# Performance work log

Measured on AMD Instinct MI355X. Metric: run time of the kernel, lower is better.

Reference implementation:

```python
import jax, jax.numpy as jnp
import numpy as np

N_ADDR, N_TX = 150000, 200000
IN_DIM, HID, HEADS = 64, 32, 4
DIM = HID // HEADS
E_AT, E_TA, E_AA = 1000000, 1000000, 500000
SLOPE = 0.2  # HANConv default negative_slope


def setup_inputs() -> dict:
    key = jax.random.key(0)
    ks = jax.random.split(key, 16)
    f = lambda k, shape, s: jax.random.normal(k, shape, dtype=jnp.float32) * s
    return {
        "x_addr": f(ks[0], (N_ADDR, IN_DIM), 1.0),
        "x_tx": f(ks[1], (N_TX, IN_DIM), 1.0),
        "e_at_src": jax.random.randint(ks[2], (E_AT,), 0, N_ADDR, dtype=jnp.int32),
        "e_at_dst": jax.random.randint(ks[3], (E_AT,), 0, N_TX, dtype=jnp.int32),
        "e_ta_src": jax.random.randint(ks[4], (E_TA,), 0, N_TX, dtype=jnp.int32),
        "e_ta_dst": jax.random.randint(ks[5], (E_TA,), 0, N_ADDR, dtype=jnp.int32),
        "e_aa_src": jax.random.randint(ks[6], (E_AA,), 0, N_ADDR, dtype=jnp.int32),
        "e_aa_dst": jax.random.randint(ks[7], (E_AA,), 0, N_ADDR, dtype=jnp.int32),
        "pW1": f(ks[8], (2, IN_DIM, HID), 0.1),      # layer-1 proj per node type [addr, tx]
        "pb1": jnp.zeros((2, HID), jnp.float32),
        "pW23": f(ks[9], (2, 2, HID, HID), 0.1),     # [layer-1, node_type]
        "pb23": jnp.zeros((2, 2, HID), jnp.float32),
        "att_src": f(ks[10], (3, 3, HEADS, DIM), 0.1),  # [layer, edge_type, H, D]
        "att_dst": f(ks[11], (3, 3, HEADS, DIM), 0.1),
        "kW": f(ks[12], (3, HID, HID), 0.1),         # semantic k_lin per layer
        "kb": jnp.zeros((3, HID), jnp.float32),
        "q": f(ks[13], (3, HID), 0.1),               # semantic query per layer
        "linW": f(ks[14], (HID, 2), 0.1),
        "linb": jnp.zeros((2,), jnp.float32),
    }


def _edge_softmax(logits, dst, n):
    # numerically stable segment softmax over destination neighborhoods
    m = jax.ops.segment_max(logits, dst, num_segments=n)          # [n, H]
    m = jnp.where(jnp.isfinite(m), m, 0.0)
    e = jnp.exp(logits - m[dst])
    s = jax.ops.segment_sum(e, dst, num_segments=n)
    return e / (s[dst] + 1e-16)


def _relation(h_src, h_dst, src, dst, a_s, a_d, n_dst):
    alpha_src = jnp.einsum('nhd,hd->nh', h_src, a_s)
    alpha_dst = jnp.einsum('nhd,hd->nh', h_dst, a_d)
    logit = alpha_src[src] + alpha_dst[dst]                        # [E, H]
    logit = jnp.where(logit >= 0, logit, SLOPE * logit)            # leaky_relu
    alpha = _edge_softmax(logit, dst, n_dst)
    msg = h_src[src] * alpha[:, :, None]                           # [E, H, D]
    out = jax.ops.segment_sum(msg, dst, num_segments=n_dst)        # [n_dst, H, D]
    return jax.nn.relu(out.reshape(n_dst, HID))


def _semantic(xs, kW, kb, q):
    # xs: [R, N, F]; semantic-level attention over R relations (PyG `group`)
    t = jnp.tanh(xs @ kW + kb).mean(axis=1)       # [R, F]
    attn = jax.nn.softmax((t * q).sum(-1))        # [R]
    return jnp.einsum('r,rnf->nf', attn, xs)


def _han_layer(x_a, x_t, Wa, ba, Wt, bt, a_s, a_d, kW, kb, q, edges):
    h_a = (x_a @ Wa + ba).reshape(-1, HEADS, DIM)
    h_t = (x_t @ Wt + bt).reshape(-1, HEADS, DIM)
    o_tx = _relation(h_a, h_t, edges[0], edges[1], a_s[0], a_d[0], N_TX)
    o_a1 = _relation(h_t, h_a, edges[2], edges[3], a_s[1], a_d[1], N_ADDR)
    o_a2 = _relation(h_a, h_a, edges[4], edges[5], a_s[2], a_d[2], N_ADDR)
    new_a = _semantic(jnp.stack([o_a1, o_a2]), kW, kb, q)
    new_t = _semantic(o_tx[None], kW, kb, q)
    return new_a, new_t


def reference(x_addr, x_tx, e_at_src, e_at_dst, e_ta_src, e_ta_dst,
              e_aa_src, e_aa_dst, pW1, pb1, pW23, pb23, att_src, att_dst,
              kW, kb, q, linW, linb):
    edges = (e_at_src, e_at_dst, e_ta_src, e_ta_dst, e_aa_src, e_aa_dst)
    a, t = _han_layer(x_addr, x_tx, pW1[0], pb1[0], pW1[1], pb1[1],
                      att_src[0], att_dst[0], kW[0], kb[0], q[0], edges)
    a, t = jax.nn.relu(a), jax.nn.relu(t)  # wrapper relu; dropout = eval identity
    for l in range(2):
        a, t = _han_layer(a, t, pW23[l, 0], pb23[l, 0], pW23[l, 1], pb23[l, 1],
                          att_src[l + 1], att_dst[l + 1],
                          kW[l + 1], kb[l + 1], q[l + 1], edges)
        a, t = jax.nn.relu(a), jax.nn.relu(t)
    return a @ linW + linb
```

## Files before the change

### kernel.cpp

```cpp
#include <hip/hip_runtime.h>
#include <hip/hip_bf16.h>
#include <hip/hip_fp16.h>

#define NA 150000
#define NT 200000
#define E_AT 1000000
#define E_TA 1000000
#define E_AA 500000

#define CHK 2048
#define CAP 8192
#define P_AT 391
#define P_TA 293
#define P_AA 293
#define NBINS (P_AT + P_TA + P_AA)
#define CB_AT 489
#define CB_TA 489
#define CB_AA 245

#define GB_AT 6250
#define GB_TA 4688
#define GB_AA 4688

#define GA32 4688
#define GT32 6250
#define NB_SEM 586

#define WO_W1   0
#define WO_B1   4096
#define WO_W23  4160
#define WO_B23  8256
#define WO_AS   8384
#define WO_AD   8672
#define WO_KW   8960
#define WO_KB   12032
#define WO_Q    12128
#define WO_LW   12224
#define WO_LB   12288
#define WT_TOT  12290

__device__ __forceinline__ float ldf(const void* p, long i, int f32) {
    if (f32) return ((const float*)p)[i];
    unsigned int u = ((const unsigned short*)p)[i];
    union { unsigned int ui; float f; } v; v.ui = u << 16;
    return v.f;
}
__device__ __forceinline__ float bf2f(unsigned short u) {
    union { unsigned int ui; float f; } v; v.ui = ((unsigned int)u) << 16;
    return v.f;
}
__device__ __forceinline__ float h2f(unsigned short u) {
    return __half2float(__ushort_as_half(u));
}
__device__ __forceinline__ unsigned short f2h(float x) {
    return __half_as_ushort(__float2half(x));
}
__device__ __forceinline__ float ftanh(float x) {
    x = fminf(fmaxf(x, -9.f), 9.f);
    float e = __expf(2.f * x);
    return (e - 1.f) / (e + 1.f);
}

__global__ void k_init(const void* __restrict__ x,
                       const void* __restrict__ pW1, const void* __restrict__ pb1,
                       const void* __restrict__ pW23, const void* __restrict__ pb23,
                       const void* __restrict__ attS, const void* __restrict__ attD,
                       const void* __restrict__ kW, const void* __restrict__ kb,
                       const void* __restrict__ qv, const void* __restrict__ linW,
                       const void* __restrict__ linb,
                       float* __restrict__ wts, int* __restrict__ flagp,
                       int* __restrict__ gcnt) {
    __shared__ int cnt;
    const int t = threadIdx.x;
    if (t == 0) cnt = 0;
    __syncthreads();
    const unsigned short* u = (const unsigned short*)x;
    int wild = 0;
    for (int i = t; i < 4096; i += 256) {
        unsigned short v = u[i];
        int e = (v >> 7) & 0xFF;
        if (e > 133 || (e != 0 && e < 100)) wild++;
        else if (e == 0 && (v & 0x7F)) wild++;
    }
    atomicAdd(&cnt, wild);
    __syncthreads();
    const int f32 = (cnt > 1024) ? 1 : 0;
    if (t == 0) *flagp = f32;
    for (int i = t; i < 1024; i += 256) gcnt[i] = 0;
    for (int i = t; i < 4096; i += 256) wts[WO_W1 + i]  = ldf(pW1, i, f32);
    for (int i = t; i < 64;   i += 256) wts[WO_B1 + i]  = ldf(pb1, i, f32);
    for (int i = t; i < 4096; i += 256) wts[WO_W23 + i] = ldf(pW23, i, f32);
    for (int i = t; i < 128;  i += 256) wts[WO_B23 + i] = ldf(pb23, i, f32);
    for (int i = t; i < 288;  i += 256) wts[WO_AS + i]  = ldf(attS, i, f32);
    for (int i = t; i < 288;  i += 256) wts[WO_AD + i]  = ldf(attD, i, f32);
    for (int i = t; i < 3072; i += 256) wts[WO_KW + i]  = ldf(kW, i, f32);
    for (int i = t; i < 96;   i += 256) wts[WO_KB + i]  = ldf(kb, i, f32);
    for (int i = t; i < 96;   i += 256) wts[WO_Q + i]   = ldf(qv, i, f32);
    for (int i = t; i < 64;   i += 256) wts[WO_LW + i]  = ldf(linW, i, f32);
    for (int i = t; i < 2;    i += 256) wts[WO_LB + i]  = ldf(linb, i, f32);
}

template<int K, int LMODE>
__global__ __launch_bounds__(256) void k_proj2(
        const void* __restrict__ Xa, const void* __restrict__ Xt,
        const void* __restrict__ X2, const float* __restrict__ attn,
        const float* __restrict__ W, int wOffA, int wOffT,
        const float* __restrict__ Bv, int bOffA, int bOffT,
        unsigned short* __restrict__ Ha, unsigned short* __restrict__ Ht,
        const float* __restrict__ attD, int lBase,
        float* __restrict__ ad0, float* __restrict__ ad1, float* __restrict__ ad2,
        const int* __restrict__ flagp, float* __restrict__ zsem) {
    constexpr int XS = K + 4;
    constexpr int CPR = K / 4;
    constexpr int TOT4 = 32 * CPR;
    __shared__ float Xs[32 * XS];
    __shared__ float Wl[K * 32];
    const int t = threadIdx.x;
    if (blockIdx.x == 0 && t < 64) zsem[t] = 0.f;
    const bool isA = blockIdx.x < GA32;
    const int bb = isA ? (int)blockIdx.x : (int)blockIdx.x - GA32;
    const int N = isA ? NA : NT;
    const int wOff = isA ? wOffA : wOffT;
    const int bOff = isA ? bOffA : bOffT;
    const long n0 = (long)bb * 32;
    for (int i = t; i < K * 32; i += 256) Wl[i] = W[wOff + i];
    if (LMODE == 1) {
        if (isA) {
            const float w0 = attn[0], w1 = attn[1];
            const float* A1 = (const float*)Xa;
            const float* A2 = (const float*)X2;
            for (int i = t; i < TOT4; i += 256) {
                int r = i / CPR, c = (i - r * CPR) * 4;
                long gr = n0 + r; if (gr >= N) gr = N - 1;
                float4 va = *(const float4*)&A1[gr * K + c];
                float4 vb = *(const float4*)&A2[gr * K + c];
                float4 o;
                o.x = fmaxf(w0 * va.x + w1 * vb.x, 0.f);
                o.y = fmaxf(w0 * va.y + w1 * vb.y, 0.f);
                o.z = fmaxf(w0 * va.z + w1 * vb.z, 0.f);
                o.w = fmaxf(w0 * va.w + w1 * vb.w, 0.f);
                *(float4*)&Xs[r * XS + c] = o;
            }
        } else {
            const float* Xf = (const float*)Xt;
            for (int i = t; i < TOT4; i += 256) {
                int r = i / CPR, c = (i - r * CPR) * 4;
                long gr = n0 + r; if (gr >= N) gr = N - 1;
                *(float4*)&Xs[r * XS + c] = *(const float4*)&Xf[gr * K + c];
            }
        }
    } else {
        const void* X = isA ? Xa : Xt;
        const int f32 = *flagp;
        if (f32) {
            const float* Xf = (const float*)X;
            for (int i = t; i < TOT4; i += 256) {
                int r = i / CPR, c = (i - r * CPR) * 4;
                long gr = n0 + r; if (gr >= N) gr = N - 1;
                *(float4*)&Xs[r * XS + c] = *(const float4*)&Xf[gr * K + c];
            }
        } else {
            const unsigned short* Xh = (const unsigned short*)X;
            for (int i = t; i < TOT4; i += 256) {
                int r = i / CPR, c = (i - r * CPR) * 4;
                long gr = n0 + r; if (gr >= N) gr = N - 1;
                ushort4 v = *(const ushort4*)&Xh[gr * K + c];
                float4 o;
                o.x = bf2f(v.x); o.y = bf2f(v.y); o.z = bf2f(v.z); o.w = bf2f(v.w);
                *(float4*)&Xs[r * XS + c] = o;
            }
        }
    }
    __syncthreads();
    const int g = t >> 3;
    const int q = t & 7;
    const long n = n0 + g;
    float a0 = Bv[bOff + q * 4 + 0];
    float a1 = Bv[bOff + q * 4 + 1];
    float a2 = Bv[bOff + q * 4 + 2];
    float a3 = Bv[bOff + q * 4 + 3];
#pragma unroll 4
    for (int k4 = 0; k4 < K; k4 += 4) {
        float4 xv = *(const float4*)&Xs[g * XS + k4];
        float4 w0 = *(const float4*)&Wl[(k4 + 0) * 32 + q * 4];
        float4 w1 = *(const float4*)&Wl[(k4 + 1) * 32 + q * 4];
        float4 w2 = *(const float4*)&Wl[(k4 + 2) * 32 + q * 4];
        float4 w3 = *(const float4*)&Wl[(k4 + 3) * 32 + q * 4];
        a0 = fmaf(xv.x, w0.x, a0); a1 = fmaf(xv.x, w0.y, a1);
        a2 = fmaf(xv.x, w0.z, a2); a3 = fmaf(xv.x, w0.w, a3);
        a0 = fmaf(xv.y, w1.x, a0); a1 = fmaf(xv.y, w1.y, a1);
        a2 = fmaf(xv.y, w1.z, a2); a3 = fmaf(xv.y, w1.w, a3);
        a0 = fmaf(xv.z, w2.x, a0); a1 = fmaf(xv.z, w2.y, a1);
        a2 = fmaf(xv.z, w2.z, a2); a3 = fmaf(xv.z, w2.w, a3);
        a0 = fmaf(xv.w, w3.x, a0); a1 = fmaf(xv.w, w3.y, a1);
        a2 = fmaf(xv.w, w3.z, a2); a3 = fmaf(xv.w, w3.w, a3);
    }
    if (n < N) {
        unsigned short* Hh = isA ? Ha : Ht;
        unsigned int p01 = (unsigned)f2h(a0) | ((unsigned)f2h(a1) << 16);
        unsigned int p23 = (unsigned)f2h(a2) | ((unsigned)f2h(a3) << 16);
        *(uint2*)&Hh[n * 32 + q * 4] = make_uint2(p01, p23);
        const int hh = q >> 1;
        const int ai = lBase + q * 4;
        if (isA) {
            float p1 = a0 * attD[ai + 32] + a1 * attD[ai + 33]
                     + a2 * attD[ai + 34] + a3 * attD[ai + 35];
            float p2 = a0 * attD[ai + 64] + a1 * attD[ai + 65]
                     + a2 * attD[ai + 66] + a3 * attD[ai + 67];
            float s1 = p1 + __shfl_xor(p1, 1);
            float s2 = p2 + __shfl_xor(p2, 1);
            if (!(q & 1)) { ad1[n * 4 + hh] = s1; ad2[n * 4 + hh] = s2; }
        } else {
            float p0 = a0 * attD[ai] + a1 * attD[ai + 1]
                     + a2 * attD[ai + 2] + a3 * attD[ai + 3];
            float s0 = p0 + __shfl_xor(p0, 1);
            if (!(q & 1)) ad0[n * 4 + hh] = s0;
        }
    }
}

__global__ __launch_bounds__(256) void k_bin(
        const int* __restrict__ eat_s, const int* __restrict__ eat_d,
        const int* __restrict__ eta_s, const int* __restrict__ eta_d,
        const int* __restrict__ eaa_s, const int* __restrict__ eaa_d,
        int* __restrict__ gcnt,
        int* __restrict__ slot_at, int* __restrict__ slot_ta, int* __restrict__ slot_aa) {
    __shared__ int hist[P_AT];
    int b = blockIdx.x, t = threadIdx.x;
    const int *src, *dst; int E, P, seg; int* slot;
    if (b < CB_AT)              { src = eat_s; dst = eat_d; E = E_AT; P = P_AT; seg = 0;            slot = slot_at; }
    else if (b < CB_AT + CB_TA) { b -= CB_AT;  src = eta_s; dst = eta_d; E = E_TA; P = P_TA; seg = P_AT;        slot = slot_ta; }
    else                        { b -= CB_AT + CB_TA; src = eaa_s; dst = eaa_d; E = E_AA; P = P_AA; seg = P_AT + P_TA; slot = slot_aa; }
    long e0 = (long)b * CHK;
    for (int i = t; i < P; i += 256) hist[i] = 0;
    __syncthreads();
    for (int k = 0; k < CHK; k += 256) {
        long e = e0 + k + t;
        if (e < E) atomicAdd(&hist[dst[e] >> 9], 1);
    }
    __syncthreads();
    for (int i = t; i < P; i += 256) {
        int v = hist[i];
        hist[i] = atomicAdd(&gcnt[seg + i], v);
    }
    __syncthreads();
    for (int k = 0; k < CHK; k += 256) {
        long e = e0 + k + t;
        if (e < E) {
            int d = dst[e];
            int bin = d >> 9;
            int pos = atomicAdd(&hist[bin], 1);
            slot[bin * CAP + pos] = ((d & 511) << 18) | src[e];
        }
    }
}

__global__ void k_binscan(const int* __restrict__ gcnt, int* __restrict__ bbase,
                          int* __restrict__ off_at, int* __restrict__ off_ta,
                          int* __restrict__ off_aa) {
    __shared__ int sa[512], sb[512];
    int t = threadIdx.x;
    const int segs[4] = {0, P_AT, P_AT + P_TA, NBINS};
    for (int r = 0; r < 3; r++) {
        int s0 = segs[r], P = segs[r + 1] - s0;
        sa[t] = (t < P) ? gcnt[s0 + t] : 0;
        __syncthreads();
        int* in = sa; int* out = sb;
        for (int o = 1; o < 512; o <<= 1) {
            out[t] = in[t] + (t >= o ? in[t - o] : 0);
            __syncthreads();
            int* tmp = in; in = out; out = tmp;
        }
        if (t < P) bbase[s0 + t] = (t ? in[t - 1] : 0);
        __syncthreads();
    }
    if (t == 0) { off_at[NT] = E_AT; off_ta[NA] = E_TA; off_aa[NA] = E_AA; }
}

__global__ __launch_bounds__(256) void k_binsort(
        const int* __restrict__ gcnt, const int* __restrict__ bbase,
        const int* __restrict__ slot_at, const int* __restrict__ slot_ta,
        const int* __restrict__ slot_aa,
        int* __restrict__ off_at, int* __restrict__ off_ta, int* __restrict__ off_aa,
        int* __restrict__ csr_at, int* __restrict__ csr_ta, int* __restrict__ csr_aa) {
    __shared__ int sa[512], sb[512], cur[512];
    int b = blockIdx.x, t = threadIdx.x;
    const int* slot; int* off; int* csr; int N, bin, seg;
    if (b < P_AT)              { slot = slot_at; off = off_at; csr = csr_at; N = NT; bin = b;                seg = 0; }
    else if (b < P_AT + P_TA)  { slot = slot_ta; off = off_ta; csr = csr_ta; N = NA; bin = b - P_AT;         seg = P_AT; }
    else                       { slot = slot_aa; off = off_aa; csr = csr_aa; N = NA; bin = b - P_AT - P_TA;  seg = P_AT + P_TA; }
    const int cnt  = gcnt[seg + bin];
    const int base = bbase[seg + bin];
    const int* sp = &slot[bin * CAP];
    sa[t] = 0; sa[t + 256] = 0;
    __syncthreads();
    for (int i = t; i < cnt; i += 256) atomicAdd(&sa[sp[i] >> 18], 1);
    __syncthreads();
    int* in = sa; int* out = sb;
    for (int o = 1; o < 512; o <<= 1) {
        for (int i = t; i < 512; i += 256)
            out[i] = in[i] + (i >= o ? in[i - o] : 0);
        __syncthreads();
        int* tmp = in; in = out; out = tmp;
    }
    for (int i = t; i < 512; i += 256) {
        int excl = i ? in[i - 1] : 0;
        cur[i] = excl;
        int gd = bin * 512 + i;
        if (gd < N) off[gd] = base + excl;
    }
    __syncthreads();
    for (int i = t; i < cnt; i += 256) {
        int pk = sp[i];
        int pos = atomicAdd(&cur[pk >> 18], 1);
        csr[base + pos] = pk & 0x3FFFF;
    }
}

__global__ __launch_bounds__(256) void k_gather3(
        const int* __restrict__ off_at, const int* __restrict__ csr_at,
        const int* __restrict__ off_ta, const int* __restrict__ csr_ta,
        const int* __restrict__ off_aa, const int* __restrict__ csr_aa,
        const float* __restrict__ ad0, const float* __restrict__ ad1,
        const float* __restrict__ ad2,
        const unsigned short* __restrict__ h_a, const unsigned short* __restrict__ h_t,
        float* __restrict__ o_tx, float* __restrict__ o_a1, float* __restrict__ o_a2,
        const float* __restrict__ attS, int lBase) {
    int b = blockIdx.x;
    const int *off, *csr;
    const float *ad_;
    const unsigned short* Hs;
    float* O;
    int N, attOff;
    if (b < GB_AT) {
        off = off_at; csr = csr_at; ad_ = ad0; Hs = h_a; O = o_tx; N = NT;
        attOff = lBase;
    } else if (b < GB_AT + GB_TA) {
        b -= GB_AT;
        off = off_ta; csr = csr_ta; ad_ = ad1; Hs = h_t; O = o_a1; N = NA;
        attOff = lBase + 32;
    } else {
        b -= GB_AT + GB_TA;
        off = off_aa; csr = csr_aa; ad_ = ad2; Hs = h_a; O = o_a2; N = NA;
        attOff = lBase + 64;
    }
    const int t = threadIdx.x;
    const int q = t & 7;
    const int hh = q >> 1;
    const int n = b * 32 + (t >> 3);
    if (n >= N) return;
    const float4 aq = *(const float4*)&attS[attOff + q * 4];
    const float aq0 = aq.x, aq1 = aq.y, aq2 = aq.z, aq3 = aq.w;
    const float adv = ad_[n * 4 + hh];
    const int p0 = off[n], p1 = off[n + 1];
    float ax = 0.f, ay = 0.f, az = 0.f, aw = 0.f, se = 0.f;
    int p = p0;
    for (; p + 4 <= p1; p += 4) {
        int s0 = csr[p], s1 = csr[p + 1], s2 = csr[p + 2], s3 = csr[p + 3];
        ushort4 v0 = *(const ushort4*)&Hs[s0 * 32 + q * 4];
        ushort4 v1 = *(const ushort4*)&Hs[s1 * 32 + q * 4];
        ushort4 v2 = *(const ushort4*)&Hs[s2 * 32 + q * 4];
        ushort4 v3 = *(const ushort4*)&Hs[s3 * 32 + q * 4];
        float h00 = h2f(v0.x), h01 = h2f(v0.y), h02 = h2f(v0.z), h03 = h2f(v0.w);
        float h10 = h2f(v1.x), h11 = h2f(v1.y), h12 = h2f(v1.z), h13 = h2f(v1.w);
        float h20 = h2f(v2.x), h21 = h2f(v2.y), h22 = h2f(v2.z), h23 = h2f(v2.w);
        float h30 = h2f(v3.x), h31 = h2f(v3.y), h32 = h2f(v3.z), h33 = h2f(v3.w);
        float pt0 = h00 * aq0 + h01 * aq1 + h02 * aq2 + h03 * aq3;
        float pt1 = h10 * aq0 + h11 * aq1 + h12 * aq2 + h13 * aq3;
        float pt2 = h20 * aq0 + h21 * aq1 + h22 * aq2 + h23 * aq3;
        float pt3 = h30 * aq0 + h31 * aq1 + h32 * aq2 + h33 * aq3;
        float al0 = pt0 + __shfl_xor(pt0, 1);
        float al1 = pt1 + __shfl_xor(pt1, 1);
        float al2 = pt2 + __shfl_xor(pt2, 1);
        float al3 = pt3 + __shfl_xor(pt3, 1);
        float l0 = al0 + adv; l0 = fmaxf(l0, 0.2f * l0); float e0 = __expf(l0);
        float l1 = al1 + adv; l1 = fmaxf(l1, 0.2f * l1); float e1 = __expf(l1);
        float l2 = al2 + adv; l2 = fmaxf(l2, 0.2f * l2); float e2 = __expf(l2);
        float l3 = al3 + adv; l3 = fmaxf(l3, 0.2f * l3); float e3 = __expf(l3);
        se += e0 + e1 + e2 + e3;
        ax += e0 * h00 + e1 * h10 + e2 * h20 + e3 * h30;
        ay += e0 * h01 + e1 * h11 + e2 * h21 + e3 * h31;
        az += e0 * h02 + e1 * h12 + e2 * h22 + e3 * h32;
        aw += e0 * h03 + e1 * h13 + e2 * h23 + e3 * h33;
    }
    for (; p < p1; p++) {
        int s = csr[p];
        ushort4 v = *(const ushort4*)&Hs[s * 32 + q * 4];
        float h0 = h2f(v.x), h1 = h2f(v.y), h2 = h2f(v.z), h3 = h2f(v.w);
        float pt = h0 * aq0 + h1 * aq1 + h2 * aq2 + h3 * aq3;
        float al = pt + __shfl_xor(pt, 1);
        float l = al + adv; l = fmaxf(l, 0.2f * l);
        float e = __expf(l);
        se += e;
        ax += e * h0; ay += e * h1; az += e * h2; aw += e * h3;
    }
    const float inv = 1.f / (se + 1e-16f);
    float4 r;
    r.x = fmaxf(ax * inv, 0.f);
    r.y = fmaxf(ay * inv, 0.f);
    r.z = fmaxf(az * inv, 0.f);
    r.w = fmaxf(aw * inv, 0.f);
    *(float4*)&O[n * 32 + q * 4] = r;
}

__global__ __launch_bounds__(256) void k_sem_reduce2(
        const float* __restrict__ O1, const float* __restrict__ O2,
        const float* __restrict__ kWl, const float* __restrict__ kbl,
        float* __restrict__ accum) {
    __shared__ float w[1056];
    __shared__ float sacc[32];
    const int r = (blockIdx.x >= NB_SEM) ? 1 : 0;
    const float* O = r ? O2 : O1;
    for (int i = threadIdx.x; i < 1024; i += 256) w[i] = kWl[i];
    if (threadIdx.x < 32) {
        w[1024 + threadIdx.x] = kbl[threadIdx.x];
        sacc[threadIdx.x] = 0.f;
    }
    __syncthreads();
    long n = (long)(blockIdx.x - r * NB_SEM) * 256 + threadIdx.x;
    float y[32];
    if (n < NA) {
        float x[32];
#pragma unroll
        for (int k = 0; k < 32; k++) x[k] = O[n * 32 + k];
#pragma unroll
        for (int f = 0; f < 32; f++) {
            float acc = w[1024 + f];
#pragma unroll
            for (int k = 0; k < 32; k++) acc += x[k] * w[k * 32 + f];
            y[f] = ftanh(acc);
        }
    } else {
#pragma unroll
        for (int f = 0; f < 32; f++) y[f] = 0.f;
    }
#pragma unroll
    for (int f = 0; f < 32; f++) {
        float v = y[f];
        for (int o = 32; o > 0; o >>= 1) v += __shfl_xor(v, o, 64);
        if ((threadIdx.x & 63) == 0) atomicAdd(&sacc[f], v);
    }
    __syncthreads();
    if (threadIdx.x < 32) atomicAdd(&accum[r * 32 + threadIdx.x], sacc[threadIdx.x]);
}

__global__ void k_sem_attn(const float* __restrict__ accum, float Ninv,
                           const float* __restrict__ q, float* __restrict__ attn) {
    if (threadIdx.x == 0) {
        float s0 = 0.f, s1 = 0.f;
        for (int f = 0; f < 32; f++) {
            float qf = q[f];
            s0 += accum[f] * Ninv * qf;
            s1 += accum[32 + f] * Ninv * qf;
        }
        float m = fmaxf(s0, s1);
        float e0 = __expf(s0 - m), e1 = __expf(s1 - m);
        float inv = 1.f / (e0 + e1);
        attn[0] = e0 * inv;
        attn[1] = e1 * inv;
    }
}

__global__ void k_combine_final(const float* __restrict__ o1, const float* __restrict__ o2,
                                const float* __restrict__ attn,
                                const float* __restrict__ linW, const float* __restrict__ linb,
                                void* __restrict__ out, int N, const int* __restrict__ flagp) {
    int n = blockIdx.x * blockDim.x + threadIdx.x;
    if (n >= N) return;
    int f32 = *flagp;
    float w0 = attn[0], w1 = attn[1];
    float s0 = linb[0], s1 = linb[1];
    const float* p1 = &o1[(long)n * 32];
    const float* p2 = &o2[(long)n * 32];
#pragma unroll
    for (int f = 0; f < 32; f++) {
        float v = w0 * p1[f] + w1 * p2[f];
        v = (v > 0.f) ? v : 0.f;
        s0 += v * linW[f * 2];
        s1 += v * linW[f * 2 + 1];
    }
    if (f32) { ((float*)out)[n * 2] = s0; ((float*)out)[n * 2 + 1] = s1; }
    else {
        ((__hip_bfloat16*)out)[n * 2] = __float2bfloat16(s0);
        ((__hip_bfloat16*)out)[n * 2 + 1] = __float2bfloat16(s1);
    }
}

static inline int gblocks(long n) { return (int)((n + 255) / 256); }

extern "C" void kernel_launch(void* const* d_in, const int* in_sizes, int n_in,
                              void* d_out, int out_size, void* d_ws, size_t ws_size,
                              hipStream_t stream) {
    const void* x_addr = d_in[0];
    const void* x_tx   = d_in[1];
    const int* eat_s = (const int*)d_in[2];
    const int* eat_d = (const int*)d_in[3];
    const int* eta_s = (const int*)d_in[4];
    const int* eta_d = (const int*)d_in[5];
    const int* eaa_s = (const int*)d_in[6];
    const int* eaa_d = (const int*)d_in[7];
    const void* pW1  = d_in[8];
    const void* pb1  = d_in[9];
    const void* pW23 = d_in[10];
    const void* pb23 = d_in[11];
    const void* attS = d_in[12];
    const void* attD = d_in[13];
    const void* kW   = d_in[14];
    const void* kb   = d_in[15];
    const void* qv   = d_in[16];
    const void* linW = d_in[17];
    const void* linb = d_in[18];

    const size_t NA32 = (size_t)NA * 32, NT32 = (size_t)NT * 32;
    const size_t NA4 = (size_t)NA * 4, NT4 = (size_t)NT * 4;

    float* ws    = (float*)d_ws;
    float* h_aF  = ws;
    float* h_tF  = h_aF + NA32;
    float* o_a1  = h_tF + NT32;
    float* o_a2  = o_a1 + NA32;
    float* o_tx  = o_a2 + NA32;
    float* ad1   = o_tx + NT32;
    float* ad2   = ad1 + NA4;
    float* ad0   = ad2 + NA4;
    float* sem   = ad0 + NT4;
    int*   flagp = (int*)(sem + 66);
    int*   off_at = flagp + 16;
    int*   off_ta = off_at + (NT + 1);
    int*   off_aa = off_ta + (NA + 1);
    int*   csr_at = off_aa + (NA + 1);
    int*   csr_ta = csr_at + E_AT;
    int*   csr_aa = csr_ta + E_TA;
    int*   gcnt   = csr_aa + E_AA;
    int*   bbase  = gcnt + 1024;
    int*   slot_at = bbase + 1024;
    int*   slot_ta = slot_at + P_AT * CAP;
    int*   slot_aa = slot_ta + P_TA * CAP;
    float* wts    = (float*)(slot_aa + (size_t)P_AA * CAP);

    unsigned short* h_a = (unsigned short*)h_aF;
    unsigned short* h_t = (unsigned short*)h_tF;

    k_init<<<1, 256, 0, stream>>>(x_addr, pW1, pb1, pW23, pb23, attS, attD,
                                  kW, kb, qv, linW, linb, wts, flagp, gcnt);

    k_bin<<<CB_AT + CB_TA + CB_AA, 256, 0, stream>>>(
        eat_s, eat_d, eta_s, eta_d, eaa_s, eaa_d, gcnt, slot_at, slot_ta, slot_aa);
    k_binscan<<<1, 512, 0, stream>>>(gcnt, bbase, off_at, off_ta, off_aa);
    k_binsort<<<NBINS, 256, 0, stream>>>(gcnt, bbase, slot_at, slot_ta, slot_aa,
                                         off_at, off_ta, off_aa, csr_at, csr_ta, csr_aa);

    for (int l = 0; l < 3; l++) {
        if (l == 0) {
            k_proj2<64, 0><<<GA32 + GT32, 256, 0, stream>>>(
                x_addr, x_tx, nullptr, sem + 64,
                wts + WO_W1, 0, 2048, wts + WO_B1, 0, 32,
                h_a, h_t, wts + WO_AD, 0, ad0, ad1, ad2, flagp, sem);
        } else {
            int wi = (l - 1) * 2;
            k_proj2<32, 1><<<GA32 + GT32, 256, 0, stream>>>(
                o_a1, o_tx, o_a2, sem + 64,
                wts + WO_W23, (wi + 0) * 1024, (wi + 1) * 1024,
                wts + WO_B23, (wi + 0) * 32, (wi + 1) * 32,
                h_a, h_t, wts + WO_AD, l * 96, ad0, ad1, ad2, flagp, sem);
        }
        k_gather3<<<GB_AT + GB_TA + GB_AA, 256, 0, stream>>>(
            off_at, csr_at, off_ta, csr_ta, off_aa, csr_aa,
            ad0, ad1, ad2, h_a, h_t, o_tx, o_a1, o_a2, wts + WO_AS, l * 96);
        k_sem_reduce2<<<2 * NB_SEM, 256, 0, stream>>>(
            o_a1, o_a2, wts + WO_KW + l * 1024, wts + WO_KB + l * 32, sem);
        k_sem_attn<<<1, 64, 0, stream>>>(sem, 1.0f / NA, wts + WO_Q + l * 32, sem + 64);
        if (l == 2) {
            k_combine_final<<<gblocks(NA), 256, 0, stream>>>(o_a1, o_a2, sem + 64,
                                                             wts + WO_LW, wts + WO_LB,
                                                             d_out, NA, flagp);
        }
    }
}
```

Before: 662.4 us.

## Fuse semantic attention into gather and edge binning into layer-1 projection

After: 780.9 us. +17.9%, slower.

```diff
diff --git a/kernel.cpp b/kernel.cpp
--- a/kernel.cpp
+++ b/kernel.cpp
@@ -8,15 +8,16 @@
 #define E_TA 1000000
 #define E_AA 500000
 
-#define CHK 2048
+#define CHK 4096
 #define CAP 8192
 #define P_AT 391
 #define P_TA 293
 #define P_AA 293
 #define NBINS (P_AT + P_TA + P_AA)
-#define CB_AT 489
-#define CB_TA 489
-#define CB_AA 245
+#define CB_AT 245
+#define CB_TA 245
+#define CB_AA 123
+#define NBBIN (CB_AT + CB_TA + CB_AA)
 
 #define GB_AT 6250
 #define GB_TA 4688
@@ -24,7 +25,6 @@
 
 #define GA32 4688
 #define GT32 6250
-#define NB_SEM 586
 
 #define WO_W1   0
 #define WO_B1   4096
@@ -37,7 +37,6 @@
 #define WO_Q    12128
 #define WO_LW   12224
 #define WO_LB   12288
-#define WT_TOT  12290
 
 __device__ __forceinline__ float ldf(const void* p, long i, int f32) {
     if (f32) return ((const float*)p)[i];
@@ -69,7 +68,7 @@
                        const void* __restrict__ qv, const void* __restrict__ linW,
                        const void* __restrict__ linb,
                        float* __restrict__ wts, int* __restrict__ flagp,
-                       int* __restrict__ gcnt) {
+                       int* __restrict__ gcnt, float* __restrict__ sem) {
     __shared__ int cnt;
     const int t = threadIdx.x;
     if (t == 0) cnt = 0;
@@ -86,6 +85,7 @@
     __syncthreads();
     const int f32 = (cnt > 1024) ? 1 : 0;
     if (t == 0) *flagp = f32;
+    if (t < 8) sem[t] = 0.f;
     for (int i = t; i < 1024; i += 256) gcnt[i] = 0;
     for (int i = t; i < 4096; i += 256) wts[WO_W1 + i]  = ldf(pW1, i, f32);
     for (int i = t; i < 64;   i += 256) wts[WO_B1 + i]  = ldf(pb1, i, f32);
@@ -100,56 +100,63 @@
     for (int i = t; i < 2;    i += 256) wts[WO_LB + i]  = ldf(linb, i, f32);
 }
 
-template<int K, int LMODE>
-__global__ __launch_bounds__(256) void k_proj2(
+__global__ __launch_bounds__(256) void k_projbin(
         const void* __restrict__ Xa, const void* __restrict__ Xt,
-        const void* __restrict__ X2, const float* __restrict__ attn,
-        const float* __restrict__ W, int wOffA, int wOffT,
-        const float* __restrict__ Bv, int bOffA, int bOffT,
+        const float* __restrict__ W, const float* __restrict__ Bv,
         unsigned short* __restrict__ Ha, unsigned short* __restrict__ Ht,
-        const float* __restrict__ attD, int lBase,
+        const float* __restrict__ attD,
         float* __restrict__ ad0, float* __restrict__ ad1, float* __restrict__ ad2,
-        const int* __restrict__ flagp, float* __restrict__ zsem) {
-    constexpr int XS = K + 4;
-    constexpr int CPR = K / 4;
-    constexpr int TOT4 = 32 * CPR;
-    __shared__ float Xs[32 * XS];
-    __shared__ float Wl[K * 32];
+        const int* __restrict__ flagp,
+        const int* __restrict__ eat_s, const int* __restrict__ eat_d,
+        const int* __restrict__ eta_s, const int* __restrict__ eta_d,
+        const int* __restrict__ eaa_s, const int* __restrict__ eaa_d,
+        int* __restrict__ gcnt,
+        int* __restrict__ slot_at, int* __restrict__ slot_ta, int* __restrict__ slot_aa) {
+    __shared__ float smem[4224];
     const int t = threadIdx.x;
-    if (blockIdx.x == 0 && t < 64) zsem[t] = 0.f;
-    const bool isA = blockIdx.x < GA32;
-    const int bb = isA ? (int)blockIdx.x : (int)blockIdx.x - GA32;
+    int b = blockIdx.x;
+    if (b < NBBIN) {
+        int* hist = (int*)smem;
+        const int *src, *dst; int E, P, seg; int* slot;
+        if (b < CB_AT)              { src = eat_s; dst = eat_d; E = E_AT; P = P_AT; seg = 0;            slot = slot_at; }
+        else if (b < CB_AT + CB_TA) { b -= CB_AT;  src = eta_s; dst = eta_d; E = E_TA; P = P_TA; seg = P_AT;        slot = slot_ta; }
+        else                        { b -= CB_AT + CB_TA; src = eaa_s; dst = eaa_d; E = E_AA; P = P_AA; seg = P_AT + P_TA; slot = slot_aa; }
+        long e0 = (long)b * CHK;
+        for (int i = t; i < P; i += 256) hist[i] = 0;
+        __syncthreads();
+        for (int k = 0; k < CHK; k += 256) {
+            long e = e0 + k + t;
+            if (e < E) atomicAdd(&hist[dst[e] >> 9], 1);
+        }
+        __syncthreads();
+        for (int i = t; i < P; i += 256) {
+            int v = hist[i];
+            hist[i] = atomicAdd(&gcnt[seg + i], v);
+        }
+        __syncthreads();
+        for (int k = 0; k < CHK; k += 256) {
+            long e = e0 + k + t;
+            if (e < E) {
+                int d = dst[e];
+                int bin = d >> 9;
+                int pos = atomicAdd(&hist[bin], 1);
+                slot[bin * CAP + pos] = ((d & 511) << 18) | src[e];
+            }
+        }
+        return;
+    }
+    b -= NBBIN;
+    constexpr int K = 64, XS = K + 4, CPR = K / 4, TOT4 = 32 * CPR;
+    float* Xs = smem;
+    float* Wl = smem + 2176;
+    const bool isA = b < GA32;
+    const int bb = isA ? b : b - GA32;
     const int N = isA ? NA : NT;
-    const int wOff = isA ? wOffA : wOffT;
-    const int bOff = isA ? bOffA : bOffT;
+    const int wOff = isA ? 0 : 2048;
+    const int bOff = isA ? 0 : 32;
     const long n0 = (long)bb * 32;
     for (int i = t; i < K * 32; i += 256) Wl[i] = W[wOff + i];
-    if (LMODE == 1) {
-        if (isA) {
-            const float w0 = attn[0], w1 = attn[1];
-            const float* A1 = (const float*)Xa;
-            const float* A2 = (const float*)X2;
-            for (int i = t; i < TOT4; i += 256) {
-                int r = i / CPR, c = (i - r * CPR) * 4;
-                long gr = n0 + r; if (gr >= N) gr = N - 1;
-                float4 va = *(const float4*)&A1[gr * K + c];
-                float4 vb = *(const float4*)&A2[gr * K + c];
-                float4 o;
-                o.x = fmaxf(w0 * va.x + w1 * vb.x, 0.f);
-                o.y = fmaxf(w0 * va.y + w1 * vb.y, 0.f);
-                o.z = fmaxf(w0 * va.z + w1 * vb.z, 0.f);
-                o.w = fmaxf(w0 * va.w + w1 * vb.w, 0.f);
-                *(float4*)&Xs[r * XS + c] = o;
-            }
-        } else {
-            const float* Xf = (const float*)Xt;
-            for (int i = t; i < TOT4; i += 256) {
-                int r = i / CPR, c = (i - r * CPR) * 4;
-                long gr = n0 + r; if (gr >= N) gr = N - 1;
-                *(float4*)&Xs[r * XS + c] = *(const float4*)&Xf[gr * K + c];
-            }
-        }
-    } else {
+    {
         const void* X = isA ? Xa : Xt;
         const int f32 = *flagp;
         if (f32) {
@@ -172,8 +179,7 @@
         }
     }
     __syncthreads();
-    const int g = t >> 3;
-    const int q = t & 7;
+    const int g = t >> 3, q = t & 7;
     const long n = n0 + g;
     float a0 = Bv[bOff + q * 4 + 0];
     float a1 = Bv[bOff + q * 4 + 1];
@@ -201,6 +207,97 @@
         unsigned int p23 = (unsigned)f2h(a2) | ((unsigned)f2h(a3) << 16);
         *(uint2*)&Hh[n * 32 + q * 4] = make_uint2(p01, p23);
         const int hh = q >> 1;
+        const int ai = q * 4;
+        if (isA) {
+            float p1 = a0 * attD[ai + 32] + a1 * attD[ai + 33]
+                     + a2 * attD[ai + 34] + a3 * attD[ai + 35];
+            float p2 = a0 * attD[ai + 64] + a1 * attD[ai + 65]
+                     + a2 * attD[ai + 66] + a3 * attD[ai + 67];
+            float s1 = p1 + __shfl_xor(p1, 1);
+            float s2 = p2 + __shfl_xor(p2, 1);
+            if (!(q & 1)) { ad1[n * 4 + hh] = s1; ad2[n * 4 + hh] = s2; }
+        } else {
+            float p0 = a0 * attD[ai] + a1 * attD[ai + 1]
+                     + a2 * attD[ai + 2] + a3 * attD[ai + 3];
+            float s0 = p0 + __shfl_xor(p0, 1);
+            if (!(q & 1)) ad0[n * 4 + hh] = s0;
+        }
+    }
+}
+
+__global__ __launch_bounds__(256) void k_proj2(
+        const float* __restrict__ O1, const float* __restrict__ Ot,
+        const float* __restrict__ O2, const float* __restrict__ semL,
+        const float* __restrict__ W, int wOffA, int wOffT,
+        const float* __restrict__ Bv, int bOffA, int bOffT,
+        unsigned short* __restrict__ Ha, unsigned short* __restrict__ Ht,
+        const float* __restrict__ attD, int lBase,
+        float* __restrict__ ad0, float* __restrict__ ad1, float* __restrict__ ad2) {
+    constexpr int K = 32, XS = K + 4, CPR = K / 4, TOT4 = 32 * CPR;
+    __shared__ float Xs[32 * XS];
+    __shared__ float Wl[K * 32];
+    const int t = threadIdx.x;
+    const bool isA = blockIdx.x < GA32;
+    const int bb = isA ? (int)blockIdx.x : (int)blockIdx.x - GA32;
+    const int N = isA ? NA : NT;
+    const int wOff = isA ? wOffA : wOffT;
+    const int bOff = isA ? bOffA : bOffT;
+    const long n0 = (long)bb * 32;
+    for (int i = t; i < K * 32; i += 256) Wl[i] = W[wOff + i];
+    if (isA) {
+        float s0 = semL[0] * (1.0f / NA), s1 = semL[1] * (1.0f / NA);
+        float m = fmaxf(s0, s1);
+        float e0 = __expf(s0 - m), e1 = __expf(s1 - m);
+        float inv = 1.f / (e0 + e1);
+        const float w0 = e0 * inv, w1 = e1 * inv;
+        for (int i = t; i < TOT4; i += 256) {
+            int r = i / CPR, c = (i - r * CPR) * 4;
+            long gr = n0 + r; if (gr >= N) gr = N - 1;
+            float4 va = *(const float4*)&O1[gr * K + c];
+            float4 vb = *(const float4*)&O2[gr * K + c];
+            float4 o;
+            o.x = fmaxf(w0 * va.x + w1 * vb.x, 0.f);
+            o.y = fmaxf(w0 * va.y + w1 * vb.y, 0.f);
+            o.z = fmaxf(w0 * va.z + w1 * vb.z, 0.f);
+            o.w = fmaxf(w0 * va.w + w1 * vb.w, 0.f);
+            *(float4*)&Xs[r * XS + c] = o;
+        }
+    } else {
+        for (int i = t; i < TOT4; i += 256) {
+            int r = i / CPR, c = (i - r * CPR) * 4;
+            long gr = n0 + r; if (gr >= N) gr = N - 1;
+            *(float4*)&Xs[r * XS + c] = *(const float4*)&Ot[gr * K + c];
+        }
+    }
+    __syncthreads();
+    const int g = t >> 3, q = t & 7;
+    const long n = n0 + g;
+    float a0 = Bv[bOff + q * 4 + 0];
+    float a1 = Bv[bOff + q * 4 + 1];
+    float a2 = Bv[bOff + q * 4 + 2];
+    float a3 = Bv[bOff + q * 4 + 3];
+#pragma unroll 4
+    for (int k4 = 0; k4 < K; k4 += 4) {
+        float4 xv = *(const float4*)&Xs[g * XS + k4];
+        float4 w0 = *(const float4*)&Wl[(k4 + 0) * 32 + q * 4];
+        float4 w1 = *(const float4*)&Wl[(k4 + 1) * 32 + q * 4];
+        float4 w2 = *(const float4*)&Wl[(k4 + 2) * 32 + q * 4];
+        float4 w3 = *(const float4*)&Wl[(k4 + 3) * 32 + q * 4];
+        a0 = fmaf(xv.x, w0.x, a0); a1 = fmaf(xv.x, w0.y, a1);
+        a2 = fmaf(xv.x, w0.z, a2); a3 = fmaf(xv.x, w0.w, a3);
+        a0 = fmaf(xv.y, w1.x, a0); a1 = fmaf(xv.y, w1.y, a1);
+        a2 = fmaf(xv.y, w1.z, a2); a3 = fmaf(xv.y, w1.w, a3);
+        a0 = fmaf(xv.z, w2.x, a0); a1 = fmaf(xv.z, w2.y, a1);
+        a2 = fmaf(xv.z, w2.z, a2); a3 = fmaf(xv.z, w2.w, a3);
+        a0 = fmaf(xv.w, w3.x, a0); a1 = fmaf(xv.w, w3.y, a1);
+        a2 = fmaf(xv.w, w3.z, a2); a3 = fmaf(xv.w, w3.w, a3);
+    }
+    if (n < N) {
+        unsigned short* Hh = isA ? Ha : Ht;
+        unsigned int p01 = (unsigned)f2h(a0) | ((unsigned)f2h(a1) << 16);
+        unsigned int p23 = (unsigned)f2h(a2) | ((unsigned)f2h(a3) << 16);
+        *(uint2*)&Hh[n * 32 + q * 4] = make_uint2(p01, p23);
+        const int hh = q >> 1;
         const int ai = lBase + q * 4;
         if (isA) {
             float p1 = a0 * attD[ai + 32] + a1 * attD[ai + 33]
@@ -215,42 +312,6 @@
                      + a2 * attD[ai + 2] + a3 * attD[ai + 3];
             float s0 = p0 + __shfl_xor(p0, 1);
             if (!(q & 1)) ad0[n * 4 + hh] = s0;
-        }
-    }
-}
-
-__global__ __launch_bounds__(256) void k_bin(
-        const int* __restrict__ eat_s, const int* __restrict__ eat_d,
-        const int* __restrict__ eta_s, const int* __restrict__ eta_d,
-        const int* __restrict__ eaa_s, const int* __restrict__ eaa_d,
-        int* __restrict__ gcnt,
-        int* __restrict__ slot_at, int* __restrict__ slot_ta, int* __restrict__ slot_aa) {
-    __shared__ int hist[P_AT];
-    int b = blockIdx.x, t = threadIdx.x;
-    const int *src, *dst; int E, P, seg; int* slot;
-    if (b < CB_AT)              { src = eat_s; dst = eat_d; E = E_AT; P = P_AT; seg = 0;            slot = slot_at; }
-    else if (b < CB_AT + CB_TA) { b -= CB_AT;  src = eta_s; dst = eta_d; E = E_TA; P = P_TA; seg = P_AT;        slot = slot_ta; }
-    else                        { b -= CB_AT + CB_TA; src = eaa_s; dst = eaa_d; E = E_AA; P = P_AA; seg = P_AT + P_TA; slot = slot_aa; }
-    long e0 = (long)b * CHK;
-    for (int i = t; i < P; i += 256) hist[i] = 0;
-    __syncthreads();
-    for (int k = 0; k < CHK; k += 256) {
-        long e = e0 + k + t;
-        if (e < E) atomicAdd(&hist[dst[e] >> 9], 1);
-    }
-    __syncthreads();
-    for (int i = t; i < P; i += 256) {
-        int v = hist[i];
-        hist[i] = atomicAdd(&gcnt[seg + i], v);
-    }
-    __syncthreads();
-    for (int k = 0; k < CHK; k += 256) {
-        long e = e0 + k + t;
-        if (e < E) {
-            int d = dst[e];
-            int bin = d >> 9;
-            int pos = atomicAdd(&hist[bin], 1);
-            slot[bin * CAP + pos] = ((d & 511) << 18) | src[e];
         }
     }
 }
@@ -325,150 +386,136 @@
         const float* __restrict__ ad2,
         const unsigned short* __restrict__ h_a, const unsigned short* __restrict__ h_t,
         float* __restrict__ o_tx, float* __restrict__ o_a1, float* __restrict__ o_a2,
-        const float* __restrict__ attS, int lBase) {
+        const float* __restrict__ attS, int lBase,
+        const float* __restrict__ kWl, const float* __restrict__ kbl,
+        const float* __restrict__ qvl, float* __restrict__ semL) {
+    __shared__ float kws[1088];
+    __shared__ float bacc;
     int b = blockIdx.x;
     const int *off, *csr;
     const float *ad_;
     const unsigned short* Hs;
     float* O;
-    int N, attOff;
+    int N, attOff, rel;
     if (b < GB_AT) {
         off = off_at; csr = csr_at; ad_ = ad0; Hs = h_a; O = o_tx; N = NT;
-        attOff = lBase;
+        attOff = lBase; rel = 0;
     } else if (b < GB_AT + GB_TA) {
         b -= GB_AT;
         off = off_ta; csr = csr_ta; ad_ = ad1; Hs = h_t; O = o_a1; N = NA;
-        attOff = lBase + 32;
+        attOff = lBase + 32; rel = 1;
     } else {
         b -= GB_AT + GB_TA;
         off = off_aa; csr = csr_aa; ad_ = ad2; Hs = h_a; O = o_a2; N = NA;
-        attOff = lBase + 64;
+        attOff = lBase + 64; rel = 2;
     }
     const int t = threadIdx.x;
+    if (t == 0) bacc = 0.f;
+    if (rel) {
+        for (int i = t; i < 1024; i += 256) kws[i] = kWl[i];
+        if (t < 32) kws[1024 + t] = kbl[t];
+        if (t >= 64 && t < 96) kws[1056 + (t - 64)] = qvl[t - 64];
+    }
+    __syncthreads();
     const int q = t & 7;
     const int hh = q >> 1;
     const int n = b * 32 + (t >> 3);
-    if (n >= N) return;
-    const float4 aq = *(const float4*)&attS[attOff + q * 4];
-    const float aq0 = aq.x, aq1 = aq.y, aq2 = aq.z, aq3 = aq.w;
-    const float adv = ad_[n * 4 + hh];
-    const int p0 = off[n], p1 = off[n + 1];
-    float ax = 0.f, ay = 0.f, az = 0.f, aw = 0.f, se = 0.f;
-    int p = p0;
-    for (; p + 4 <= p1; p += 4) {
-        int s0 = csr[p], s1 = csr[p + 1], s2 = csr[p + 2], s3 = csr[p + 3];
-        ushort4 v0 = *(const ushort4*)&Hs[s0 * 32 + q * 4];
-        ushort4 v1 = *(const ushort4*)&Hs[s1 * 32 + q * 4];
-        ushort4 v2 = *(const ushort4*)&Hs[s2 * 32 + q * 4];
-        ushort4 v3 = *(const ushort4*)&Hs[s3 * 32 + q * 4];
-        float h00 = h2f(v0.x), h01 = h2f(v0.y), h02 = h2f(v0.z), h03 = h2f(v0.w);
-        float h10 = h2f(v1.x), h11 = h2f(v1.y), h12 = h2f(v1.z), h13 = h2f(v1.w);
-        float h20 = h2f(v2.x), h21 = h2f(v2.y), h22 = h2f(v2.z), h23 = h2f(v2.w);
-        float h30 = h2f(v3.x), h31 = h2f(v3.y), h32 = h2f(v3.z), h33 = h2f(v3.w);
-        float pt0 = h00 * aq0 + h01 * aq1 + h02 * aq2 + h03 * aq3;
-        float pt1 = h10 * aq0 + h11 * aq1 + h12 * aq2 + h13 * aq3;
-        float pt2 = h20 * aq0 + h21 * aq1 + h22 * aq2 + h23 * aq3;
-        float pt3 = h30 * aq0 + h31 * aq1 + h32 * aq2 + h33 * aq3;
-        float al0 = pt0 + __shfl_xor(pt0, 1);
-        float al1 = pt1 + __shfl_xor(pt1, 1);
-        float al2 = pt2 + __shfl_xor(pt2, 1);
-        float al3 = pt3 + __shfl_xor(pt3, 1);
-        float l0 = al0 + adv; l0 = fmaxf(l0, 0.2f * l0); float e0 = __expf(l0);
-        float l1 = al1 + adv; l1 = fmaxf(l1, 0.2f * l1); float e1 = __expf(l1);
-        float l2 = al2 + adv; l2 = fmaxf(l2, 0.2f * l2); float e2 = __expf(l2);
-        float l3 = al3 + adv; l3 = fmaxf(l3, 0.2f * l3); float e3 = __expf(l3);
-        se += e0 + e1 + e2 + e3;
-        ax += e0 * h00 + e1 * h10 + e2 * h20 + e3 * h30;
-        ay += e0 * h01 + e1 * h11 + e2 * h21 + e3 * h31;
-        az += e0 * h02 + e1 * h12 + e2 * h22 + e3 * h32;
-        aw += e0 * h03 + e1 * h13 + e2 * h23 + e3 * h33;
-    }
-    for (; p < p1; p++) {
-        int s = csr[p];
-        ushort4 v = *(const ushort4*)&Hs[s * 32 + q * 4];
-        float h0 = h2f(v.x), h1 = h2f(v.y), h2 = h2f(v.z), h3 = h2f(v.w);
-        float pt = h0 * aq0 + h1 * aq1 + h2 * aq2 + h3 * aq3;
-        float al = pt + __shfl_xor(pt, 1);
-        float l = al + adv; l = fmaxf(l, 0.2f * l);
-        float e = __expf(l);
-        se += e;
-        ax += e * h0; ay += e * h1; az += e * h2; aw += e * h3;
-    }
-    const float inv = 1.f / (se + 1e-16f);
-    float4 r;
-    r.x = fmaxf(ax * inv, 0.f);
-    r.y = fmaxf(ay * inv, 0.f);
-    r.z = fmaxf(az * inv, 0.f);
-    r.w = fmaxf(aw * inv, 0.f);
-    *(float4*)&O[n * 32 + q * 4] = r;
-}
-
-__global__ __launch_bounds__(256) void k_sem_reduce2(
-        const float* __restrict__ O1, const float* __restrict__ O2,
-        const float* __restrict__ kWl, const float* __restrict__ kbl,
-        float* __restrict__ accum) {
-    __shared__ float w[1056];
-    __shared__ float sacc[32];
-    const int r = (blockIdx.x >= NB_SEM) ? 1 : 0;
-    const float* O = r ? O2 : O1;
-    for (int i = threadIdx.x; i < 1024; i += 256) w[i] = kWl[i];
-    if (threadIdx.x < 32) {
-        w[1024 + threadIdx.x] = kbl[threadIdx.x];
-        sacc[threadIdx.x] = 0.f;
-    }
-    __syncthreads();
-    long n = (long)(blockIdx.x - r * NB_SEM) * 256 + threadIdx.x;
-    float y[32];
-    if (n < NA) {
-        float x[32];
+    if (n < N) {
+        const float4 aq = *(const float4*)&attS[attOff + q * 4];
+        const float aq0 = aq.x, aq1 = aq.y, aq2 = aq.z, aq3 = aq.w;
+        const float adv = ad_[n * 4 + hh];
+        const int p0 = off[n], p1 = off[n + 1];
+        float ax = 0.f, ay = 0.f, az = 0.f, aw = 0.f, se = 0.f;
+        int p = p0;
+        for (; p + 4 <= p1; p += 4) {
+            int s0 = csr[p], s1 = csr[p + 1], s2 = csr[p + 2], s3 = csr[p + 3];
+            ushort4 v0 = *(const ushort4*)&Hs[s0 * 32 + q * 4];
+            ushort4 v1 = *(const ushort4*)&Hs[s1 * 32 + q * 4];
+            ushort4 v2 = *(const ushort4*)&Hs[s2 * 32 + q * 4];
+            ushort4 v3 = *(const ushort4*)&Hs[s3 * 32 + q * 4];
+            float h00 = h2f(v0.x), h01 = h2f(v0.y), h02 = h2f(v0.z), h03 = h2f(v0.w);
+            float h10 = h2f(v1.x), h11 = h2f(v1.y), h12 = h2f(v1.z), h13 = h2f(v1.w);
+            float h20 = h2f(v2.x), h21 = h2f(v2.y), h22 = h2f(v2.z), h23 = h2f(v2.w);
+            float h30 = h2f(v3.x), h31 = h2f(v3.y), h32 = h2f(v3.z), h33 = h2f(v3.w);
+            float pt0 = h00 * aq0 + h01 * aq1 + h02 * aq2 + h03 * aq3;
+            float pt1 = h10 * aq0 + h11 * aq1 + h12 * aq2 + h13 * aq3;
+            float pt2 = h20 * aq0 + h21 * aq1 + h22 * aq2 + h23 * aq3;
+            float pt3 = h30 * aq0 + h31 * aq1 + h32 * aq2 + h33 * aq3;
+            float al0 = pt0 + __shfl_xor(pt0, 1);
+            float al1 = pt1 + __shfl_xor(pt1, 1);
+            float al2 = pt2 + __shfl_xor(pt2, 1);
+            float al3 = pt3 + __shfl_xor(pt3, 1);
+            float l0 = al0 + adv; l0 = fmaxf(l0, 0.2f * l0); float e0 = __expf(l0);
+            float l1 = al1 + adv; l1 = fmaxf(l1, 0.2f * l1); float e1 = __expf(l1);
+            float l2 = al2 + adv; l2 = fmaxf(l2, 0.2f * l2); float e2 = __expf(l2);
+            float l3 = al3 + adv; l3 = fmaxf(l3, 0.2f * l3); float e3 = __expf(l3);
+            se += e0 + e1 + e2 + e3;
+            ax += e0 * h00 + e1 * h10 + e2 * h20 + e3 * h30;
+            ay += e0 * h01 + e1 * h11 + e2 * h21 + e3 * h31;
+            az += e0 * h02 + e1 * h12 + e2 * h22 + e3 * h32;
+            aw += e0 * h03 + e1 * h13 + e2 * h23 + e3 * h33;
+        }
+        for (; p < p1; p++) {
+            int s = csr[p];
+            ushort4 v = *(const ushort4*)&Hs[s * 32 + q * 4];
+            float h0 = h2f(v.x), h1 = h2f(v.y), h2 = h2f(v.z), h3 = h2f(v.w);
+            float pt = h0 * aq0 + h1 * aq1 + h2 * aq2 + h3 * aq3;
+            float al = pt + __shfl_xor(pt, 1);
+            float l = al + adv; l = fmaxf(l, 0.2f * l);
+            float e = __expf(l);
+            se += e;
+            ax += e * h0; ay += e * h1; az += e * h2; aw += e * h3;
+        }
+        const float inv = 1.f / (se + 1e-16f);
+        float4 r;
+        r.x = fmaxf(ax * inv, 0.f);
+        r.y = fmaxf(ay * inv, 0.f);
+        r.z = fmaxf(az * inv, 0.f);
+        r.w = fmaxf(aw * inv, 0.f);
+        *(float4*)&O[n * 32 + q * 4] = r;
+        if (rel) {
+            float S0 = 0.f, S1 = 0.f, S2 = 0.f, S3 = 0.f;
+            const int fb = q * 4;
 #pragma unroll
-        for (int k = 0; k < 32; k++) x[k] = O[n * 32 + k];
-#pragma unroll
-        for (int f = 0; f < 32; f++) {
-            float acc = w[1024 + f];
-#pragma unroll
-            for (int k = 0; k < 32; k++) acc += x[k] * w[k * 32 + f];
-            y[f] = ftanh(acc);
-        }
-    } else {
-#pragma unroll
-        for (int f = 0; f < 32; f++) y[f] = 0.f;
-    }
-#pragma unroll
-    for (int f = 0; f < 32; f++) {
-        float v = y[f];
-        for (int o = 32; o > 0; o >>= 1) v += __shfl_xor(v, o, 64);
-        if ((threadIdx.x & 63) == 0) atomicAdd(&sacc[f], v);
-    }
-    __syncthreads();
-    if (threadIdx.x < 32) atomicAdd(&accum[r * 32 + threadIdx.x], sacc[threadIdx.x]);
-}
-
-__global__ void k_sem_attn(const float* __restrict__ accum, float Ninv,
-                           const float* __restrict__ q, float* __restrict__ attn) {
-    if (threadIdx.x == 0) {
-        float s0 = 0.f, s1 = 0.f;
-        for (int f = 0; f < 32; f++) {
-            float qf = q[f];
-            s0 += accum[f] * Ninv * qf;
-            s1 += accum[32 + f] * Ninv * qf;
-        }
-        float m = fmaxf(s0, s1);
-        float e0 = __expf(s0 - m), e1 = __expf(s1 - m);
-        float inv = 1.f / (e0 + e1);
-        attn[0] = e0 * inv;
-        attn[1] = e1 * inv;
-    }
+            for (int s = 0; s < 8; s++) {
+                float o0 = __shfl_xor(r.x, s);
+                float o1 = __shfl_xor(r.y, s);
+                float o2 = __shfl_xor(r.z, s);
+                float o3 = __shfl_xor(r.w, s);
+                const int pb = (q ^ s) * 128 + fb;
+                S0 += o0 * kws[pb + 0] + o1 * kws[pb + 32] + o2 * kws[pb + 64] + o3 * kws[pb + 96];
+                S1 += o0 * kws[pb + 1] + o1 * kws[pb + 33] + o2 * kws[pb + 65] + o3 * kws[pb + 97];
+                S2 += o0 * kws[pb + 2] + o1 * kws[pb + 34] + o2 * kws[pb + 66] + o3 * kws[pb + 98];
+                S3 += o0 * kws[pb + 3] + o1 * kws[pb + 35] + o2 * kws[pb + 67] + o3 * kws[pb + 99];
+            }
+            float y0 = ftanh(S0 + kws[1024 + fb + 0]);
+            float y1 = ftanh(S1 + kws[1024 + fb + 1]);
+            float y2 = ftanh(S2 + kws[1024 + fb + 2]);
+            float y3 = ftanh(S3 + kws[1024 + fb + 3]);
+            float sd = y0 * kws[1056 + fb + 0] + y1 * kws[1056 + fb + 1]
+                     + y2 * kws[1056 + fb + 2] + y3 * kws[1056 + fb + 3];
+            sd += __shfl_xor(sd, 1);
+            sd += __shfl_xor(sd, 2);
+            sd += __shfl_xor(sd, 4);
+            if (q == 0) atomicAdd(&bacc, sd);
+        }
+    }
+    __syncthreads();
+    if (rel && t == 0) atomicAdd(&semL[rel - 1], bacc);
 }
 
 __global__ void k_combine_final(const float* __restrict__ o1, const float* __restrict__ o2,
-                                const float* __restrict__ attn,
+                                const float* __restrict__ semL,
                                 const float* __restrict__ linW, const float* __restrict__ linb,
                                 void* __restrict__ out, int N, const int* __restrict__ flagp) {
     int n = blockIdx.x * blockDim.x + threadIdx.x;
     if (n >= N) return;
     int f32 = *flagp;
-    float w0 = attn[0], w1 = attn[1];
+    float q0 = semL[0] * (1.0f / NA), q1 = semL[1] * (1.0f / NA);
+    float m = fmaxf(q0, q1);
+    float e0 = __expf(q0 - m), e1 = __expf(q1 - m);
+    float ai = 1.f / (e0 + e1);
+    float w0 = e0 * ai, w1 = e1 * ai;
     float s0 = linb[0], s1 = linb[1];
     const float* p1 = &o1[(long)n * 32];
     const float* p2 = &o2[(long)n * 32];
@@ -524,7 +571,7 @@
     float* ad2   = ad1 + NA4;
     float* ad0   = ad2 + NA4;
     float* sem   = ad0 + NT4;
-    int*   flagp = (int*)(sem + 66);
+    int*   flagp = (int*)(sem + 8);
     int*   off_at = flagp + 16;
     int*   off_ta = off_at + (NT + 1);
     int*   off_aa = off_ta + (NA + 1);
@@ -542,36 +589,33 @@
     unsigned short* h_t = (unsigned short*)h_tF;
 
     k_init<<<1, 256, 0, stream>>>(x_addr, pW1, pb1, pW23, pb23, attS, attD,
-                                  kW, kb, qv, linW, linb, wts, flagp, gcnt);
-
-    k_bin<<<CB_AT + CB_TA + CB_AA, 256, 0, stream>>>(
-        eat_s, eat_d, eta_s, eta_d, eaa_s, eaa_d, gcnt, slot_at, slot_ta, slot_aa);
+                                  kW, kb, qv, linW, linb, wts, flagp, gcnt, sem);
+
+    k_projbin<<<NBBIN + GA32 + GT32, 256, 0, stream>>>(
+        x_addr, x_tx, wts + WO_W1, wts + WO_B1, h_a, h_t, wts + WO_AD,
+        ad0, ad1, ad2, flagp,
+        eat_s, eat_d, eta_s, eta_d, eaa_s, eaa_d,
+        gcnt, slot_at, slot_ta, slot_aa);
     k_binscan<<<1, 512, 0, stream>>>(gcnt, bbase, off_at, off_ta, off_aa);
     k_binsort<<<NBINS, 256, 0, stream>>>(gcnt, bbase, slot_at, slot_ta, slot_aa,
                                          off_at, off_ta, off_aa, csr_at, csr_ta, csr_aa);
 
     for (int l = 0; l < 3; l++) {
-        if (l == 0) {
-            k_proj2<64, 0><<<GA32 + GT32, 256, 0, stream>>>(
-                x_addr, x_tx, nullptr, sem + 64,
-                wts + WO_W1, 0, 2048, wts + WO_B1, 0, 32,
-                h_a, h_t, wts + WO_AD, 0, ad0, ad1, ad2, flagp, sem);
-        } else {
+        if (l > 0) {
             int wi = (l - 1) * 2;
-            k_proj2<32, 1><<<GA32 + GT32, 256, 0, stream>>>(
-                o_a1, o_tx, o_a2, sem + 64,
+            k_proj2<<<GA32 + GT32, 256, 0, stream>>>(
+                o_a1, o_tx, o_a2, sem + 2 * (l - 1),
                 wts + WO_W23, (wi + 0) * 1024, (wi + 1) * 1024,
                 wts + WO_B23, (wi + 0) * 32, (wi + 1) * 32,
-                h_a, h_t, wts + WO_AD, l * 96, ad0, ad1, ad2, flagp, sem);
+                h_a, h_t, wts + WO_AD, l * 96, ad0, ad1, ad2);
         }
         k_gather3<<<GB_AT + GB_TA + GB_AA, 256, 0, stream>>>(
             off_at, csr_at, off_ta, csr_ta, off_aa, csr_aa,
-            ad0, ad1, ad2, h_a, h_t, o_tx, o_a1, o_a2, wts + WO_AS, l * 96);
-        k_sem_reduce2<<<2 * NB_SEM, 256, 0, stream>>>(
-            o_a1, o_a2, wts + WO_KW + l * 1024, wts + WO_KB + l * 32, sem);
-        k_sem_attn<<<1, 64, 0, stream>>>(sem, 1.0f / NA, wts + WO_Q + l * 32, sem + 64);
+            ad0, ad1, ad2, h_a, h_t, o_tx, o_a1, o_a2, wts + WO_AS, l * 96,
+            wts + WO_KW + l * 1024, wts + WO_KB + l * 32, wts + WO_Q + l * 32,
+            sem + 2 * l);
         if (l == 2) {
-            k_combine_final<<<gblocks(NA), 256, 0, stream>>>(o_a1, o_a2, sem + 64,
+            k_combine_final<<<gblocks(NA), 256, 0, stream>>>(o_a1, o_a2, sem + 4,
                                                              wts + WO_LW, wts + WO_LB,
                                                              d_out, NA, flagp);
         }
```
